# Optimization experiments

Measured on AMD Instinct MI355X. Metric: run time of the kernel, lower is better.

Reference implementation:

```python
import jax, jax.numpy as jnp
import numpy as np

EPS = 1e-5   # torch BatchNorm2d default eps
HEADS = 4


def conv1x1_bn(x, w, g, b, m, v):
    # 1x1 conv (no bias) == channel matmul, then inference-mode BatchNorm
    y = jnp.einsum('oc,bchw->bohw', w, x)
    s = g / jnp.sqrt(v + EPS)
    return y * s[None, :, None, None] + (b - m * s)[None, :, None, None]


def dwconv3x3_bn(x, w, g, b, m, v):
    # depthwise 3x3 conv, padding 1 (autopad), groups=C, then BatchNorm
    C = x.shape[1]
    y = jax.lax.conv_general_dilated(
        x, w, window_strides=(1, 1), padding=((1, 1), (1, 1)),
        dimension_numbers=('NCHW', 'OIHW', 'NCHW'), feature_group_count=C)
    s = g / jnp.sqrt(v + EPS)
    return y * s[None, :, None, None] + (b - m * s)[None, :, None, None]


def split_heads(x):
    b, c, h, w = x.shape
    hd = c // HEADS
    return x.reshape(b, HEADS, hd, h * w).transpose(0, 1, 3, 2)  # [b,heads,n,hd]


def merge_heads(x, h, w):
    b, heads, n, hd = x.shape
    return x.transpose(0, 1, 3, 2).reshape(b, heads * hd, h, w)


def setup_inputs() -> dict:
    key = jax.random.key(0)
    B, C, H, W = 4, 256, 48, 48
    ks = jax.random.split(key, 32)
    inp = {
        'q': jax.random.normal(ks[0], (B, C, H, W), jnp.float32),
        'k': jax.random.normal(ks[1], (B, C, H, W), jnp.float32),
        'v': jax.random.normal(ks[2], (B, C, H, W), jnp.float32),
    }
    i = 3
    for name in ['wq', 'wk', 'wv', 'proj']:
        inp[name + '_w'] = jax.random.normal(ks[i], (C, C), jnp.float32) * 0.02; i += 1
    inp['pe_w'] = jax.random.normal(ks[i], (C, 1, 3, 3), jnp.float32) * 0.1; i += 1
    for name in ['wq', 'wk', 'wv', 'pe', 'proj']:
        inp[name + '_g'] = jax.random.uniform(ks[i], (C,), jnp.float32, 0.5, 1.5); i += 1
        inp[name + '_b'] = jax.random.normal(ks[i], (C,), jnp.float32) * 0.1; i += 1
        inp[name + '_m'] = jax.random.normal(ks[i], (C,), jnp.float32) * 0.1; i += 1
        inp[name + '_v'] = jax.random.uniform(ks[i], (C,), jnp.float32, 0.5, 1.5); i += 1
    return inp


def reference(q, k, v,
              wq_w, wk_w, wv_w, proj_w, pe_w,
              wq_g, wq_b, wq_m, wq_v,
              wk_g, wk_b, wk_m, wk_v,
              wv_g, wv_b, wv_m, wv_v,
              pe_g, pe_b, pe_m, pe_v,
              proj_g, proj_b, proj_m, proj_v):
    H, W = q.shape[2], q.shape[3]
    qf = conv1x1_bn(q, wq_w, wq_g, wq_b, wq_m, wq_v)
    kf = conv1x1_bn(k, wk_w, wk_g, wk_b, wk_m, wk_v)
    vf = conv1x1_bn(v, wv_w, wv_g, wv_b, wv_m, wv_v)
    qh = split_heads(qf)  # [b,heads,n,hd]
    kh = split_heads(kf)
    vh = split_heads(vf)
    scale = qh.shape[-1] ** -0.5
    attn = jax.nn.softmax(jnp.einsum('bhnd,bhmd->bhnm', qh, kh) * scale, axis=-1)
    y = jnp.einsum('bhnm,bhmd->bhnd', attn, vh)
    y = merge_heads(y, H, W) + dwconv3x3_bn(merge_heads(qh, H, W), pe_w, pe_g, pe_b, pe_m, pe_v)
    return conv1x1_bn(y, proj_w, proj_g, proj_b, proj_m, proj_v)
```

## Files before the change

### kernel.cpp

```cpp
#include <hip/hip_runtime.h>
#include <math.h>

#define HEADS 4
#define HD    64
#define CCH   256
#define NB    4
#define HH    48
#define WW    48
#define NN    (HH*WW)
#define EPSBN 1e-5f
#define KSCL  0.18033688f
#define BCN   (NB*CCH*NN)
#define NSP   4

typedef unsigned short ushort_t;
typedef __attribute__((ext_vector_type(8))) short bfrag;
typedef __attribute__((ext_vector_type(4))) float f32x4;

#define MFMA __builtin_amdgcn_mfma_f32_16x16x32_bf16

static __device__ __forceinline__ ushort_t f2bf(float x) {
    unsigned int u = __float_as_uint(x);
    unsigned int r = (u + 0x7fffu + ((u >> 16) & 1u)) >> 16;
    return (ushort_t)r;
}
static __device__ __forceinline__ unsigned cvtpk(float lo, float hi) {
    unsigned r;
    asm("v_cvt_pk_bf16_f32 %0, %1, %2" : "=v"(r) : "v"(lo), "v"(hi));
    return r;
}
static __device__ __forceinline__ float bflo(unsigned u) { return __uint_as_float(u << 16); }
static __device__ __forceinline__ float bfhi(unsigned u) { return __uint_as_float(u & 0xffff0000u); }

static __device__ __forceinline__ void gload16(const void* g, void* l) {
    __builtin_amdgcn_global_load_lds(
        (const __attribute__((address_space(1))) void*)g,
        (__attribute__((address_space(3))) void*)l, 16, 0, 0);
}

struct PrepWP {
    const float* W[4];
    const float* G[4]; const float* Bb[4]; const float* Mm[4]; const float* Vv[4];
    const float* pew; const float* peg; const float* peb; const float* pem; const float* pev;
    ushort_t* W4; float* bias4; ushort_t* pw2; float* pbias; float* kmax2;
    const float* q; const float* k; const float* v; ushort_t* Xt;
};
__global__ __launch_bounds__(256)
void prep_kernel(PrepWP P)
{
    const int blk = blockIdx.x, tid = threadIdx.x;
    if (blk < 3456) {
        const int t  = blk / 1152;
        const int r  = blk % 1152;
        const int b  = r / 288;
        const int r2 = r % 288;
        const int n0 = (r2 >> 3) * 64;
        const int cb = (r2 & 7) * 32;
        const float* X = (t == 0) ? P.q : (t == 1) ? P.k : P.v;
        ushort_t* O = P.Xt + (size_t)t * BCN;
        const int lane = tid & 63;
        const int c0   = cb + (tid >> 6) * 8;
        const float* src = X + ((size_t)(b * CCH + c0) * NN + n0 + lane);
        float vv[8];
#pragma unroll
        for (int j = 0; j < 8; ++j) vv[j] = src[(size_t)j * NN];
        uint4 u;
        u.x = cvtpk(vv[0], vv[1]); u.y = cvtpk(vv[2], vv[3]);
        u.z = cvtpk(vv[4], vv[5]); u.w = cvtpk(vv[6], vv[7]);
        *(uint4*)&O[((size_t)b * NN + n0 + lane) * CCH + c0] = u;
        return;
    }
    const int wb = blk - 3456;
    if (wb == 128) {
        int c = tid;
        float s = P.peg[c] * rsqrtf(P.pev[c] + EPSBN);
        for (int tap = 0; tap < 9; ++tap)
            P.pw2[tap * CCH + c] = f2bf(P.pew[c * 9 + tap] * s);
        P.pbias[c] = P.peb[c] - P.pem[c] * s;
        if (tid < 16) P.kmax2[tid] = 0.f;
        return;
    }
    int g  = wb * 256 + tid;
    int cv = g >> 13;
    int o  = (g >> 5) & 255;
    int c8 = g & 31;
    float s  = P.G[cv][o] * rsqrtf(P.Vv[cv][o] + EPSBN);
    float s2 = (cv == 1) ? s * KSCL : s;
    const float* w = P.W[cv] + (size_t)o * CCH + c8 * 8;
    uint4 u;
    u.x = cvtpk(w[0]*s2, w[1]*s2); u.y = cvtpk(w[2]*s2, w[3]*s2);
    u.z = cvtpk(w[4]*s2, w[5]*s2); u.w = cvtpk(w[6]*s2, w[7]*s2);
    *(uint4*)&P.W4[((size_t)cv * CCH + o) * CCH + c8 * 8] = u;
    if (c8 == 0) {
        float bb = (P.Bb[cv][o] - P.Mm[cv][o] * s);
        P.bias4[cv * CCH + o] = (cv == 1) ? bb * KSCL : bb;
    }
}

template<int PROJ>
__global__ __launch_bounds__(256)
void conv_gemm(const ushort_t* __restrict__ T, const ushort_t* __restrict__ W4,
               const float* __restrict__ bias4,
               ushort_t* __restrict__ qnd, ushort_t* __restrict__ knd,
               ushort_t* __restrict__ vcn, float* __restrict__ outf,
               float* __restrict__ kmax2)
{
    __shared__ ushort_t Ts[64][264];
    __shared__ ushort_t Ws[64][264];
    const int nt = blockIdx.x, ot = blockIdx.y, z = blockIdx.z;
    const int which = PROJ ? 3 : (z >> 2);
    const int b = z & 3;
    const int tid = threadIdx.x;
    const int n0 = nt * 64, o0 = ot * 64;
    const ushort_t* Tsrc = T + (PROJ ? (size_t)0 : (size_t)which * BCN) + ((size_t)b * NN + n0) * CCH;
    const ushort_t* Wsrc = W4 + (size_t)which * CCH * CCH + (size_t)o0 * CCH;
    const float*    bias = bias4 + which * CCH;
#pragma unroll
    for (int i = 0; i < 8; ++i) {
        int idx = tid + i * 256;
        int r = idx >> 5, c16 = idx & 31;
        *(uint4*)&Ts[r][c16 * 8] = *(const uint4*)&Tsrc[(size_t)r * CCH + c16 * 8];
        *(uint4*)&Ws[r][c16 * 8] = *(const uint4*)&Wsrc[(size_t)r * CCH + c16 * 8];
    }
    __syncthreads();
    const int wv = tid >> 6, lane = tid & 63, lr = lane & 15, lg = lane >> 4;
    const int qn = (wv >> 1) * 32, qo = (wv & 1) * 32;
    f32x4 acc[2][2];
#pragma unroll
    for (int i = 0; i < 2; ++i)
#pragma unroll
        for (int j = 0; j < 2; ++j) acc[i][j] = (f32x4){0.f, 0.f, 0.f, 0.f};

    if (!PROJ && (z >> 2) < 2) {
#pragma unroll
        for (int k8 = 0; k8 < 8; ++k8) {
            const int kc = k8 * 32 + lg * 8;
            bfrag ta0 = *(const bfrag*)&Ts[qn + lr][kc];
            bfrag ta1 = *(const bfrag*)&Ts[qn + 16 + lr][kc];
            bfrag wa0 = *(const bfrag*)&Ws[qo + lr][kc];
            bfrag wa1 = *(const bfrag*)&Ws[qo + 16 + lr][kc];
            acc[0][0] = MFMA(ta0, wa0, acc[0][0], 0, 0, 0);
            acc[0][1] = MFMA(ta0, wa1, acc[0][1], 0, 0, 0);
            acc[1][0] = MFMA(ta1, wa0, acc[1][0], 0, 0, 0);
            acc[1][1] = MFMA(ta1, wa1, acc[1][1], 0, 0, 0);
        }
    } else {
#pragma unroll
        for (int k8 = 0; k8 < 8; ++k8) {
            const int kc = k8 * 32 + lg * 8;
            bfrag ta0 = *(const bfrag*)&Ts[qn + lr][kc];
            bfrag ta1 = *(const bfrag*)&Ts[qn + 16 + lr][kc];
            bfrag wa0 = *(const bfrag*)&Ws[qo + lr][kc];
            bfrag wa1 = *(const bfrag*)&Ws[qo + 16 + lr][kc];
            acc[0][0] = MFMA(wa0, ta0, acc[0][0], 0, 0, 0);
            acc[0][1] = MFMA(wa0, ta1, acc[0][1], 0, 0, 0);
            acc[1][0] = MFMA(wa1, ta0, acc[1][0], 0, 0, 0);
            acc[1][1] = MFMA(wa1, ta1, acc[1][1], 0, 0, 0);
        }
    }

    __syncthreads();
    if (!PROJ && which < 2) {
        ushort_t (*Ot)[72] = (ushort_t(*)[72])Ts;
        float bv[2] = { bias[o0 + qo + lr], bias[o0 + qo + 16 + lr] };
#pragma unroll
        for (int i = 0; i < 2; ++i)
#pragma unroll
            for (int j = 0; j < 2; ++j)
#pragma unroll
                for (int r = 0; r < 4; ++r)
                    Ot[qn + i * 16 + lg * 4 + r][qo + j * 16 + lr] = f2bf(acc[i][j][r] + bv[j]);
        __syncthreads();
        ushort_t* out = (which == 0) ? qnd : knd;
        for (int idx = tid; idx < 512; idx += 256) {
            int r = idx >> 3, sg = idx & 7;
            *(uint4*)&out[(((size_t)b * HEADS + ot) * NN + n0 + r) * HD + sg * 8] =
                *(const uint4*)&Ot[r][sg * 8];
        }
        if (which == 1 && tid < 64) {
            float s = 0.f;
#pragma unroll
            for (int j = 0; j < 8; ++j) {
                uint4 u = *(const uint4*)&Ot[tid][j * 8];
                s += bflo(u.x)*bflo(u.x) + bfhi(u.x)*bfhi(u.x);
                s += bflo(u.y)*bflo(u.y) + bfhi(u.y)*bfhi(u.y);
                s += bflo(u.z)*bflo(u.z) + bfhi(u.z)*bfhi(u.z);
                s += bflo(u.w)*bflo(u.w) + bfhi(u.w)*bfhi(u.w);
            }
            atomicMax((unsigned*)&kmax2[b * HEADS + ot], __float_as_uint(s));
        }
    } else if (!PROJ) {
        ushort_t (*Ot)[72] = (ushort_t(*)[72])Ts;
#pragma unroll
        for (int i = 0; i < 2; ++i)
#pragma unroll
            for (int r = 0; r < 4; ++r) {
                float bv = bias[o0 + qo + i * 16 + lg * 4 + r];
#pragma unroll
                for (int j = 0; j < 2; ++j)
                    Ot[qo + i * 16 + lg * 4 + r][qn + j * 16 + lr] = f2bf(acc[i][j][r] + bv);
            }
        __syncthreads();
        for (int idx = tid; idx < 512; idx += 256) {
            int r = idx >> 3, sg = idx & 7;
            *(uint4*)&vcn[((size_t)b * CCH + o0 + r) * NN + n0 + sg * 8] =
                *(const uint4*)&Ot[r][sg * 8];
        }
    } else {
        float (*Of)[68] = (float(*)[68])Ts;
#pragma unroll
        for (int i = 0; i < 2; ++i)
#pragma unroll
            for (int r = 0; r < 4; ++r) {
                float bv = bias[o0 + qo + i * 16 + lg * 4 + r];
#pragma unroll
                for (int j = 0; j < 2; ++j)
                    Of[qo + i * 16 + lg * 4 + r][qn + j * 16 + lr] = acc[i][j][r] + bv;
            }
        __syncthreads();
        for (int idx = tid; idx < 1024; idx += 256) {
            int r = idx >> 4, c4 = idx & 15;
            *(float4*)&outf[((size_t)b * CCH + o0 + r) * NN + n0 + c4 * 4] =
                *(const float4*)&Of[r][c4 * 4];
        }
    }
}

__global__ __launch_bounds__(256, 4)
void attn_kernel(const ushort_t* __restrict__ Qnd,
                 const ushort_t* __restrict__ Knd,
                 const ushort_t* __restrict__ Vcn,
                 const float* __restrict__ kmax2,
                 ushort_t* __restrict__ Op,
                 float* __restrict__ Larr)
{
    __shared__ __align__(16) char smem[40960];

    const int tid = threadIdx.x;
    const int lin0 = blockIdx.x + 18 * blockIdx.y + 288 * blockIdx.z;
    const int w    = (lin0 & 7) * 144 + (lin0 >> 3);
    const int qt = w % 18;
    const int bh = (w / 18) & 15;
    const int sp = w / 288;
    const int b = bh >> 2, h = bh & 3;
    const int lane = tid & 63, wv = tid >> 6;
    const int lr = lane & 15, lg = lane >> 4;
    const int lrow = lane >> 3, lslot = (lane & 7) ^ lrow;
    const int n0 = qt * 128;
    const size_t ndb = (size_t)(b * HEADS + h) * NN * HD;
    const size_t cnb = ((size_t)b * CCH + h * HD) * NN;

    const char* kgp = (const char*)(Knd + ndb) + (size_t)(sp * 576 + wv * 16 + lrow) * 128 + lslot * 16;
    const char* vgp = (const char*)(Vcn + cnb + sp * 576) + (size_t)(wv * 16 + lrow) * (NN * 2) + lslot * 16;
    char* kls = smem + wv * 2048;
    char* vls = smem + 16384 + wv * 2048;

#define STAGE(buf, t) do { \
    const char* kp_ = kgp + (size_t)(t) * 8192; \
    const char* vp_ = vgp + (size_t)(t) * 128; \
    char* kd_ = kls + (buf) * 8192; \
    char* vd_ = vls + (buf) * 8192; \
    gload16(kp_,              kd_); \
    gload16(kp_ + 1024,       kd_ + 1024); \
    gload16(vp_,              vd_); \
    gload16(vp_ + 8 * (NN*2), vd_ + 1024); \
} while (0)

    bfrag qb[2][2];
    {
        const ushort_t* qbase = Qnd + ndb + (size_t)(n0 + wv * 32 + lr) * HD;
        qb[0][0] = *(const bfrag*)&qbase[lg * 8];
        qb[0][1] = *(const bfrag*)&qbase[32 + lg * 8];
        qb[1][0] = *(const bfrag*)&qbase[16 * HD + lg * 8];
        qb[1][1] = *(const bfrag*)&qbase[16 * HD + 32 + lg * 8];
    }
    float m0[2];
    {
        const float kmx = sqrtf(kmax2[bh]);
#pragma unroll
        for (int qc = 0; qc < 2; ++qc) {
            const unsigned* u0 = (const unsigned*)&qb[qc][0];
            const unsigned* u1 = (const unsigned*)&qb[qc][1];
            float s = 0.f;
#pragma unroll
            for (int j = 0; j < 4; ++j) {
                float a0 = bflo(u0[j]), a1 = bfhi(u0[j]);
                float b0 = bflo(u1[j]), b1 = bfhi(u1[j]);
                s += a0*a0 + a1*a1 + b0*b0 + b1*b1;
            }
            s += __shfl_xor(s, 16);
            s += __shfl_xor(s, 32);
            m0[qc] = sqrtf(s) * kmx + 0.5f;
        }
    }
    bfrag ones_f;
    {
        short ov = (lr == 0) ? (short)0x3F80 : (short)0;
#pragma unroll
        for (int j = 0; j < 8; ++j) ones_f[j] = ov;
    }

    f32x4 o[2][4], o4[2];
#pragma unroll
    for (int qc = 0; qc < 2; ++qc) {
        o4[qc] = (f32x4){0.f, 0.f, 0.f, 0.f};
#pragma unroll
        for (int db = 0; db < 4; ++db) o[qc][db] = (f32x4){0.f, 0.f, 0.f, 0.f};
    }

    const int sw0 = (lg ^ (lr & 7)) << 4;
    const int sw1 = ((4 + lg) ^ (lr & 7)) << 4;
    char* Pw = smem + 32768 + wv * 2048;

    STAGE(0, 0);

    for (int t = 0; t < 9; ++t) {
        const int cur = t & 1;
        if (t < 8) {
            STAGE(cur ^ 1, t + 1);
            asm volatile("s_waitcnt vmcnt(4)" ::: "memory");
        } else {
            asm volatile("s_waitcnt vmcnt(0)" ::: "memory");
        }
        __builtin_amdgcn_s_barrier();
        const char* Kb = smem + cur * 8192;
        const char* Vb = smem + 16384 + cur * 8192;

        uint2 pd[2][4];
#pragma unroll
        for (int kb = 0; kb < 4; ++kb) {
            const char* krow = Kb + (kb * 16 + lr) * 128;
            bfrag ka0 = *(const bfrag*)(krow + sw0);
            bfrag ka1 = *(const bfrag*)(krow + sw1);
            __builtin_amdgcn_s_setprio(1);
            f32x4 z0 = (f32x4){-m0[0], -m0[0], -m0[0], -m0[0]};
            z0 = MFMA(ka0, qb[0][0], z0, 0, 0, 0);
            f32x4 s0 = MFMA(ka1, qb[0][1], z0, 0, 0, 0);
            f32x4 z1 = (f32x4){-m0[1], -m0[1], -m0[1], -m0[1]};
            z1 = MFMA(ka0, qb[1][0], z1, 0, 0, 0);
            f32x4 s1 = MFMA(ka1, qb[1][1], z1, 0, 0, 0);
            __builtin_amdgcn_s_setprio(0);
            pd[0][kb].x = cvtpk(exp2f(s0[0]), exp2f(s0[1]));
            pd[0][kb].y = cvtpk(exp2f(s0[2]), exp2f(s0[3]));
            pd[1][kb].x = cvtpk(exp2f(s1[0]), exp2f(s1[1]));
            pd[1][kb].y = cvtpk(exp2f(s1[2]), exp2f(s1[3]));
        }

        bfrag pb[2][2];
#pragma unroll
        for (int qc = 0; qc < 2; ++qc) {
            char* prow = Pw + lr * 128;
#pragma unroll
            for (int kb = 0; kb < 4; ++kb) {
                int slot = (2 * kb + (lg >> 1)) ^ (lr & 7);
                *(uint2*)(prow + slot * 16 + (lg & 1) * 8) = pd[qc][kb];
            }
            pb[qc][0] = *(const bfrag*)(prow + sw0);
            pb[qc][1] = *(const bfrag*)(prow + sw1);
        }

        __builtin_amdgcn_s_setprio(1);
#pragma unroll
        for (int db = 0; db < 4; ++db) {
            const char* vrow = Vb + (db * 16 + lr) * 128;
            bfrag va0 = *(const bfrag*)(vrow + sw0);
            bfrag va1 = *(const bfrag*)(vrow + sw1);
            o[0][db] = MFMA(va0, pb[0][0], o[0][db], 0, 0, 0);
            o[0][db] = MFMA(va1, pb[0][1], o[0][db], 0, 0, 0);
            o[1][db] = MFMA(va0, pb[1][0], o[1][db], 0, 0, 0);
            o[1][db] = MFMA(va1, pb[1][1], o[1][db], 0, 0, 0);
        }
        o4[0] = MFMA(ones_f, pb[0][0], o4[0], 0, 0, 0);
        o4[0] = MFMA(ones_f, pb[0][1], o4[0], 0, 0, 0);
        o4[1] = MFMA(ones_f, pb[1][0], o4[1], 0, 0, 0);
        o4[1] = MFMA(ones_f, pb[1][1], o4[1], 0, 0, 0);
        __builtin_amdgcn_s_setprio(0);

        __builtin_amdgcn_s_barrier();
    }
#undef STAGE

    if (lg == 0) {
#pragma unroll
        for (int qc = 0; qc < 2; ++qc)
            Larr[(size_t)(sp * 16 + bh) * NN + n0 + wv * 32 + qc * 16 + lr] = o4[qc][0];
    }
    unsigned (*Osb)[36] = (unsigned(*)[36])smem;
#pragma unroll
    for (int qc = 0; qc < 2; ++qc) {
        int row = wv * 32 + qc * 16 + lr;
#pragma unroll
        for (int db = 0; db < 4; ++db) {
            Osb[row][db * 8 + lg * 2 + 0] = cvtpk(o[qc][db][0], o[qc][db][1]);
            Osb[row][db * 8 + lg * 2 + 1] = cvtpk(o[qc][db][2], o[qc][db][3]);
        }
    }
    __syncthreads();
    ushort_t* opb = Op + (size_t)sp * BCN + ((size_t)b * NN + n0) * CCH + h * HD;
    for (int idx = tid; idx < 1024; idx += 256) {
        int n = idx >> 3, s4 = idx & 7;
        *(uint4*)&opb[(size_t)n * CCH + s4 * 8] = *(const uint4*)&Osb[n][s4 * 4];
    }
}

__global__ __launch_bounds__(256)
void fuse_kernel(const ushort_t* __restrict__ Op, const float* __restrict__ Larr,
                 const ushort_t* __restrict__ Qnd,
                 const ushort_t* __restrict__ pw2, const float* __restrict__ pbias,
                 ushort_t* __restrict__ yt)
{
    const int tid = threadIdx.x;
    const int b  = blockIdx.x / 288;
    const int n0 = (blockIdx.x % 288) * 8;
    const int c8 = tid & 31, ns = tid >> 5;
    const int n  = n0 + ns;
    const int h  = c8 >> 3, c0 = c8 * 8;

    const ushort_t* o0p = Op + ((size_t)b * NN + n) * CCH + c0;
    float acc[8] = {0.f, 0.f, 0.f, 0.f, 0.f, 0.f, 0.f, 0.f};
#pragma unroll
    for (int s = 0; s < NSP; ++s) {
        uint4 u = *(const uint4*)&o0p[(size_t)s * BCN];
        acc[0] += bflo(u.x); acc[1] += bfhi(u.x);
        acc[2] += bflo(u.y); acc[3] += bfhi(u.y);
        acc[4] += bflo(u.z); acc[5] += bfhi(u.z);
        acc[6] += bflo(u.w); acc[7] += bfhi(u.w);
    }
    int mi = (b * HEADS + h) * NN + n;
    float ls = 0.f;
#pragma unroll
    for (int s = 0; s < NSP; ++s) ls += Larr[(size_t)s * 16 * NN + mi];
    float rinv = 1.0f / ls;
#pragma unroll
    for (int j = 0; j < 8; ++j) acc[j] *= rinv;

    const int x = n % WW, y = n / WW;
    const ushort_t* qb = Qnd + (size_t)(b * HEADS + h) * NN * HD + (c8 & 7) * 8;
#pragma unroll
    for (int ky = 0; ky < 3; ++ky) {
        int yy = y + ky - 1;
        if (yy < 0 || yy >= HH) continue;
#pragma unroll
        for (int kx = 0; kx < 3; ++kx) {
            int xx = x + kx - 1;
            if (xx < 0 || xx >= WW) continue;
            int np = yy * WW + xx;
            uint4 qv = *(const uint4*)&qb[(size_t)np * HD];
            uint4 w4 = *(const uint4*)&pw2[(ky * 3 + kx) * CCH + c0];
            acc[0] += bflo(qv.x) * bflo(w4.x); acc[1] += bfhi(qv.x) * bfhi(w4.x);
            acc[2] += bflo(qv.y) * bflo(w4.y); acc[3] += bfhi(qv.y) * bfhi(w4.y);
            acc[4] += bflo(qv.z) * bflo(w4.z); acc[5] += bfhi(qv.z) * bfhi(w4.z);
            acc[6] += bflo(qv.w) * bflo(w4.w); acc[7] += bfhi(qv.w) * bfhi(w4.w);
        }
    }
    float4 p0 = *(const float4*)&pbias[c0];
    float4 p1 = *(const float4*)&pbias[c0 + 4];
    acc[0] += p0.x; acc[1] += p0.y; acc[2] += p0.z; acc[3] += p0.w;
    acc[4] += p1.x; acc[5] += p1.y; acc[6] += p1.z; acc[7] += p1.w;
    uint4 u;
    u.x = cvtpk(acc[0], acc[1]); u.y = cvtpk(acc[2], acc[3]);
    u.z = cvtpk(acc[4], acc[5]); u.w = cvtpk(acc[6], acc[7]);
    *(uint4*)&yt[((size_t)b * NN + n) * CCH + c0] = u;
}

extern "C" void kernel_launch(void* const* d_in, const int* in_sizes, int n_in,
                              void* d_out, int out_size, void* d_ws, size_t ws_size,
                              hipStream_t stream) {
    char* ws = (char*)d_ws;
    ushort_t* qnd  = (ushort_t*)(ws + 0);
    ushort_t* knd  = (ushort_t*)(ws + 4718592);
    ushort_t* vcn  = (ushort_t*)(ws + 9437184);
    ushort_t* Xt   = (ushort_t*)(ws + 14155776);
    ushort_t* Op   = (ushort_t*)(ws + 14155776);
    ushort_t* yt   = (ushort_t*)(ws + 4718592);
    float*    Larr = (float*)   (ws + 33030144);
    ushort_t* W4   = (ushort_t*)(ws + 33619968);
    float*    bias4= (float*)   (ws + 34144256);
    ushort_t* pw2  = (ushort_t*)(ws + 34148352);
    float*    pbias= (float*)   (ws + 34152960);
    float*    kmax2= (float*)   (ws + 34156032);

    PrepWP P;
    P.W[0] = (const float*)d_in[3]; P.W[1] = (const float*)d_in[4];
    P.W[2] = (const float*)d_in[5]; P.W[3] = (const float*)d_in[6];
    P.G[0]  = (const float*)d_in[8];  P.Bb[0] = (const float*)d_in[9];
    P.Mm[0] = (const float*)d_in[10]; P.Vv[0] = (const float*)d_in[11];
    P.G[1]  = (const float*)d_in[12]; P.Bb[1] = (const float*)d_in[13];
    P.Mm[1] = (const float*)d_in[14]; P.Vv[1] = (const float*)d_in[15];
    P.G[2]  = (const float*)d_in[16]; P.Bb[2] = (const float*)d_in[17];
    P.Mm[2] = (const float*)d_in[18]; P.Vv[2] = (const float*)d_in[19];
    P.G[3]  = (const float*)d_in[24]; P.Bb[3] = (const float*)d_in[25];
    P.Mm[3] = (const float*)d_in[26]; P.Vv[3] = (const float*)d_in[27];
    P.pew = (const float*)d_in[7];
    P.peg = (const float*)d_in[20]; P.peb = (const float*)d_in[21];
    P.pem = (const float*)d_in[22]; P.pev = (const float*)d_in[23];
    P.W4 = W4; P.bias4 = bias4; P.pw2 = pw2; P.pbias = pbias; P.kmax2 = kmax2;
    P.q = (const float*)d_in[0]; P.k = (const float*)d_in[1];
    P.v = (const float*)d_in[2]; P.Xt = Xt;

    prep_kernel<<<3585, 256, 0, stream>>>(P);

    conv_gemm<0><<<dim3(36, 4, 12), 256, 0, stream>>>(Xt, W4, bias4, qnd, knd, vcn, nullptr, kmax2);

    attn_kernel<<<dim3(18, 16, NSP), 256, 0, stream>>>(qnd, knd, vcn, kmax2, Op, Larr);

    fuse_kernel<<<1152, 256, 0, stream>>>(Op, Larr, qnd, pw2, pbias, yt);

    conv_gemm<1><<<dim3(36, 4, 4), 256, 0, stream>>>(yt, W4, bias4, nullptr, nullptr, nullptr,
                                                     (float*)d_out, nullptr);
}
```

Measured before the change: 91.89 us.

## Double attention query tile per block to reuse staged K/V tiles

Each attention block now handles 256 queries instead of 128, with each wave owning four 16-row query chunks. Every K/V tile staged into LDS therefore feeds twice as many MFMAs, halving global K/V traffic and the number of blocks (576 instead of 1152). The cost is more registers (launch bounds drop to 2 blocks per SM), 64KB of LDS, and fewer blocks to hide latency, so occupancy falls. P is now written to LDS inside the QK loop for each query chunk.

```diff
diff --git a/kernel.cpp b/kernel.cpp
--- a/kernel.cpp
+++ b/kernel.cpp
@@ -226,7 +226,7 @@
     }
 }
 
-__global__ __launch_bounds__(256, 4)
+__global__ __launch_bounds__(256, 2)
 void attn_kernel(const ushort_t* __restrict__ Qnd,
                  const ushort_t* __restrict__ Knd,
                  const ushort_t* __restrict__ Vcn,
@@ -234,19 +234,19 @@
                  ushort_t* __restrict__ Op,
                  float* __restrict__ Larr)
 {
-    __shared__ __align__(16) char smem[40960];
+    __shared__ __align__(16) char smem[65536];
 
     const int tid = threadIdx.x;
-    const int lin0 = blockIdx.x + 18 * blockIdx.y + 288 * blockIdx.z;
-    const int w    = (lin0 & 7) * 144 + (lin0 >> 3);
-    const int qt = w % 18;
-    const int bh = (w / 18) & 15;
-    const int sp = w / 288;
+    const int lin0 = blockIdx.x + 9 * blockIdx.y + 144 * blockIdx.z;
+    const int w    = (lin0 & 7) * 72 + (lin0 >> 3);
+    const int qt = w % 9;
+    const int bh = (w / 9) & 15;
+    const int sp = w / 144;
     const int b = bh >> 2, h = bh & 3;
     const int lane = tid & 63, wv = tid >> 6;
     const int lr = lane & 15, lg = lane >> 4;
     const int lrow = lane >> 3, lslot = (lane & 7) ^ lrow;
-    const int n0 = qt * 128;
+    const int n0 = qt * 256;
     const size_t ndb = (size_t)(b * HEADS + h) * NN * HD;
     const size_t cnb = ((size_t)b * CCH + h * HD) * NN;
 
@@ -266,19 +266,20 @@
     gload16(vp_ + 8 * (NN*2), vd_ + 1024); \
 } while (0)
 
-    bfrag qb[2][2];
+    bfrag qb[4][2];
     {
-        const ushort_t* qbase = Qnd + ndb + (size_t)(n0 + wv * 32 + lr) * HD;
-        qb[0][0] = *(const bfrag*)&qbase[lg * 8];
-        qb[0][1] = *(const bfrag*)&qbase[32 + lg * 8];
-        qb[1][0] = *(const bfrag*)&qbase[16 * HD + lg * 8];
-        qb[1][1] = *(const bfrag*)&qbase[16 * HD + 32 + lg * 8];
-    }
-    float m0[2];
+        const ushort_t* qbase = Qnd + ndb + (size_t)(n0 + wv * 64 + lr) * HD;
+#pragma unroll
+        for (int qc = 0; qc < 4; ++qc) {
+            qb[qc][0] = *(const bfrag*)&qbase[(size_t)qc * 16 * HD + lg * 8];
+            qb[qc][1] = *(const bfrag*)&qbase[(size_t)qc * 16 * HD + 32 + lg * 8];
+        }
+    }
+    float m0[4];
     {
         const float kmx = sqrtf(kmax2[bh]);
 #pragma unroll
-        for (int qc = 0; qc < 2; ++qc) {
+        for (int qc = 0; qc < 4; ++qc) {
             const unsigned* u0 = (const unsigned*)&qb[qc][0];
             const unsigned* u1 = (const unsigned*)&qb[qc][1];
             float s = 0.f;
@@ -300,9 +301,9 @@
         for (int j = 0; j < 8; ++j) ones_f[j] = ov;
     }
 
-    f32x4 o[2][4], o4[2];
-#pragma unroll
-    for (int qc = 0; qc < 2; ++qc) {
+    f32x4 o[4][4], o4[4];
+#pragma unroll
+    for (int qc = 0; qc < 4; ++qc) {
         o4[qc] = (f32x4){0.f, 0.f, 0.f, 0.f};
 #pragma unroll
         for (int db = 0; db < 4; ++db) o[qc][db] = (f32x4){0.f, 0.f, 0.f, 0.f};
@@ -310,7 +311,7 @@
 
     const int sw0 = (lg ^ (lr & 7)) << 4;
     const int sw1 = ((4 + lg) ^ (lr & 7)) << 4;
-    char* Pw = smem + 32768 + wv * 2048;
+    char* Pw = smem + 32768 + wv * 8192;
 
     STAGE(0, 0);
 
@@ -326,35 +327,30 @@
         const char* Kb = smem + cur * 8192;
         const char* Vb = smem + 16384 + cur * 8192;
 
-        uint2 pd[2][4];
+        __builtin_amdgcn_s_setprio(1);
 #pragma unroll
         for (int kb = 0; kb < 4; ++kb) {
             const char* krow = Kb + (kb * 16 + lr) * 128;
             bfrag ka0 = *(const bfrag*)(krow + sw0);
             bfrag ka1 = *(const bfrag*)(krow + sw1);
-            __builtin_amdgcn_s_setprio(1);
-            f32x4 z0 = (f32x4){-m0[0], -m0[0], -m0[0], -m0[0]};
-            z0 = MFMA(ka0, qb[0][0], z0, 0, 0, 0);
-            f32x4 s0 = MFMA(ka1, qb[0][1], z0, 0, 0, 0);
-            f32x4 z1 = (f32x4){-m0[1], -m0[1], -m0[1], -m0[1]};
-            z1 = MFMA(ka0, qb[1][0], z1, 0, 0, 0);
-            f32x4 s1 = MFMA(ka1, qb[1][1], z1, 0, 0, 0);
-            __builtin_amdgcn_s_setprio(0);
-            pd[0][kb].x = cvtpk(exp2f(s0[0]), exp2f(s0[1]));
-            pd[0][kb].y = cvtpk(exp2f(s0[2]), exp2f(s0[3]));
-            pd[1][kb].x = cvtpk(exp2f(s1[0]), exp2f(s1[1]));
-            pd[1][kb].y = cvtpk(exp2f(s1[2]), exp2f(s1[3]));
-        }
-
-        bfrag pb[2][2];
-#pragma unroll
-        for (int qc = 0; qc < 2; ++qc) {
-            char* prow = Pw + lr * 128;
-#pragma unroll
-            for (int kb = 0; kb < 4; ++kb) {
-                int slot = (2 * kb + (lg >> 1)) ^ (lr & 7);
-                *(uint2*)(prow + slot * 16 + (lg & 1) * 8) = pd[qc][kb];
+            const int slot = (2 * kb + (lg >> 1)) ^ (lr & 7);
+#pragma unroll
+            for (int qc = 0; qc < 4; ++qc) {
+                f32x4 z = (f32x4){-m0[qc], -m0[qc], -m0[qc], -m0[qc]};
+                z = MFMA(ka0, qb[qc][0], z, 0, 0, 0);
+                z = MFMA(ka1, qb[qc][1], z, 0, 0, 0);
+                uint2 u;
+                u.x = cvtpk(exp2f(z[0]), exp2f(z[1]));
+                u.y = cvtpk(exp2f(z[2]), exp2f(z[3]));
+                *(uint2*)(Pw + qc * 2048 + lr * 128 + slot * 16 + (lg & 1) * 8) = u;
             }
+        }
+        __builtin_amdgcn_s_setprio(0);
+
+        bfrag pb[4][2];
+#pragma unroll
+        for (int qc = 0; qc < 4; ++qc) {
+            const char* prow = Pw + qc * 2048 + lr * 128;
             pb[qc][0] = *(const bfrag*)(prow + sw0);
             pb[qc][1] = *(const bfrag*)(prow + sw1);
         }
@@ -365,15 +361,17 @@
             const char* vrow = Vb + (db * 16 + lr) * 128;
             bfrag va0 = *(const bfrag*)(vrow + sw0);
             bfrag va1 = *(const bfrag*)(vrow + sw1);
-            o[0][db] = MFMA(va0, pb[0][0], o[0][db], 0, 0, 0);
-            o[0][db] = MFMA(va1, pb[0][1], o[0][db], 0, 0, 0);
-            o[1][db] = MFMA(va0, pb[1][0], o[1][db], 0, 0, 0);
-            o[1][db] = MFMA(va1, pb[1][1], o[1][db], 0, 0, 0);
-        }
-        o4[0] = MFMA(ones_f, pb[0][0], o4[0], 0, 0, 0);
-        o4[0] = MFMA(ones_f, pb[0][1], o4[0], 0, 0, 0);
-        o4[1] = MFMA(ones_f, pb[1][0], o4[1], 0, 0, 0);
-        o4[1] = MFMA(ones_f, pb[1][1], o4[1], 0, 0, 0);
+#pragma unroll
+            for (int qc = 0; qc < 4; ++qc) {
+                o[qc][db] = MFMA(va0, pb[qc][0], o[qc][db], 0, 0, 0);
+                o[qc][db] = MFMA(va1, pb[qc][1], o[qc][db], 0, 0, 0);
+            }
+        }
+#pragma unroll
+        for (int qc = 0; qc < 4; ++qc) {
+            o4[qc] = MFMA(ones_f, pb[qc][0], o4[qc], 0, 0, 0);
+            o4[qc] = MFMA(ones_f, pb[qc][1], o4[qc], 0, 0, 0);
+        }
         __builtin_amdgcn_s_setprio(0);
 
         __builtin_amdgcn_s_barrier();
@@ -382,13 +380,13 @@
 
     if (lg == 0) {
 #pragma unroll
-        for (int qc = 0; qc < 2; ++qc)
-            Larr[(size_t)(sp * 16 + bh) * NN + n0 + wv * 32 + qc * 16 + lr] = o4[qc][0];
+        for (int qc = 0; qc < 4; ++qc)
+            Larr[(size_t)(sp * 16 + bh) * NN + n0 + wv * 64 + qc * 16 + lr] = o4[qc][0];
     }
     unsigned (*Osb)[36] = (unsigned(*)[36])smem;
 #pragma unroll
-    for (int qc = 0; qc < 2; ++qc) {
-        int row = wv * 32 + qc * 16 + lr;
+    for (int qc = 0; qc < 4; ++qc) {
+        int row = wv * 64 + qc * 16 + lr;
 #pragma unroll
         for (int db = 0; db < 4; ++db) {
             Osb[row][db * 8 + lg * 2 + 0] = cvtpk(o[qc][db][0], o[qc][db][1]);
@@ -397,7 +395,7 @@
     }
     __syncthreads();
     ushort_t* opb = Op + (size_t)sp * BCN + ((size_t)b * NN + n0) * CCH + h * HD;
-    for (int idx = tid; idx < 1024; idx += 256) {
+    for (int idx = tid; idx < 2048; idx += 256) {
         int n = idx >> 3, s4 = idx & 7;
         *(uint4*)&opb[(size_t)n * CCH + s4 * 8] = *(const uint4*)&Osb[n][s4 * 4];
     }
@@ -502,7 +500,7 @@
 
     conv_gemm<0><<<dim3(36, 4, 12), 256, 0, stream>>>(Xt, W4, bias4, qnd, knd, vcn, nullptr, kmax2);
 
-    attn_kernel<<<dim3(18, 16, NSP), 256, 0, stream>>>(qnd, knd, vcn, kmax2, Op, Larr);
+    attn_kernel<<<dim3(9, 16, NSP), 256, 0, stream>>>(qnd, knd, vcn, kmax2, Op, Larr);
 
     fuse_kernel<<<1152, 256, 0, stream>>>(Op, Larr, qnd, pw2, pbias, yt);
 
```

After: 103.6 us. 12.8% more time.

## Switch attention kernel to 32x32x16 MFMA with register-resident P via permlane32 swap

Applied to the files above, without the earlier changes.

Rewrites the attention inner loop to use 32x32x16 bf16 MFMAs instead of 16x16x32, so each wave computes scores for 32 queries against 32-key blocks. The score-to-PV operand transpose now stays in registers using v_permlane32_swap instead of a round-trip through LDS. The row sum is accumulated in scalar registers instead of a ones-vector MFMA. LDS usage drops, and redundant MFMAs and LDS traffic are removed, at the cost of more register pressure from the 16-wide accumulators.

```diff
diff --git a/kernel.cpp b/kernel.cpp
--- a/kernel.cpp
+++ b/kernel.cpp
@@ -16,8 +16,10 @@
 typedef unsigned short ushort_t;
 typedef __attribute__((ext_vector_type(8))) short bfrag;
 typedef __attribute__((ext_vector_type(4))) float f32x4;
-
-#define MFMA __builtin_amdgcn_mfma_f32_16x16x32_bf16
+typedef __attribute__((ext_vector_type(16))) float f32x16;
+
+#define MFMA   __builtin_amdgcn_mfma_f32_16x16x32_bf16
+#define MFMA32 __builtin_amdgcn_mfma_f32_32x32x16_bf16
 
 static __device__ __forceinline__ ushort_t f2bf(float x) {
     unsigned int u = __float_as_uint(x);
@@ -234,7 +236,7 @@
                  ushort_t* __restrict__ Op,
                  float* __restrict__ Larr)
 {
-    __shared__ __align__(16) char smem[40960];
+    __shared__ __align__(16) char smem[32768];
 
     const int tid = threadIdx.x;
     const int lin0 = blockIdx.x + 18 * blockIdx.y + 288 * blockIdx.z;
@@ -244,7 +246,7 @@
     const int sp = w / 288;
     const int b = bh >> 2, h = bh & 3;
     const int lane = tid & 63, wv = tid >> 6;
-    const int lr = lane & 15, lg = lane >> 4;
+    const int l31 = lane & 31, hi = lane >> 5, l7 = lane & 7;
     const int lrow = lane >> 3, lslot = (lane & 7) ^ lrow;
     const int n0 = qt * 128;
     const size_t ndb = (size_t)(b * HEADS + h) * NN * HD;
@@ -266,51 +268,35 @@
     gload16(vp_ + 8 * (NN*2), vd_ + 1024); \
 } while (0)
 
-    bfrag qb[2][2];
+    bfrag qb[4];
     {
-        const ushort_t* qbase = Qnd + ndb + (size_t)(n0 + wv * 32 + lr) * HD;
-        qb[0][0] = *(const bfrag*)&qbase[lg * 8];
-        qb[0][1] = *(const bfrag*)&qbase[32 + lg * 8];
-        qb[1][0] = *(const bfrag*)&qbase[16 * HD + lg * 8];
-        qb[1][1] = *(const bfrag*)&qbase[16 * HD + 32 + lg * 8];
-    }
-    float m0[2];
+        const ushort_t* qbase = Qnd + ndb + (size_t)(n0 + wv * 32 + l31) * HD + hi * 8;
+#pragma unroll
+        for (int ds = 0; ds < 4; ++ds)
+            qb[ds] = *(const bfrag*)&qbase[ds * 16];
+    }
+    float m0;
     {
-        const float kmx = sqrtf(kmax2[bh]);
-#pragma unroll
-        for (int qc = 0; qc < 2; ++qc) {
-            const unsigned* u0 = (const unsigned*)&qb[qc][0];
-            const unsigned* u1 = (const unsigned*)&qb[qc][1];
-            float s = 0.f;
+        float s = 0.f;
+#pragma unroll
+        for (int ds = 0; ds < 4; ++ds) {
+            const unsigned* uu = (const unsigned*)&qb[ds];
 #pragma unroll
             for (int j = 0; j < 4; ++j) {
-                float a0 = bflo(u0[j]), a1 = bfhi(u0[j]);
-                float b0 = bflo(u1[j]), b1 = bfhi(u1[j]);
-                s += a0*a0 + a1*a1 + b0*b0 + b1*b1;
-            }
-            s += __shfl_xor(s, 16);
-            s += __shfl_xor(s, 32);
-            m0[qc] = sqrtf(s) * kmx + 0.5f;
-        }
-    }
-    bfrag ones_f;
-    {
-        short ov = (lr == 0) ? (short)0x3F80 : (short)0;
-#pragma unroll
-        for (int j = 0; j < 8; ++j) ones_f[j] = ov;
-    }
-
-    f32x4 o[2][4], o4[2];
-#pragma unroll
-    for (int qc = 0; qc < 2; ++qc) {
-        o4[qc] = (f32x4){0.f, 0.f, 0.f, 0.f};
-#pragma unroll
-        for (int db = 0; db < 4; ++db) o[qc][db] = (f32x4){0.f, 0.f, 0.f, 0.f};
-    }
-
-    const int sw0 = (lg ^ (lr & 7)) << 4;
-    const int sw1 = ((4 + lg) ^ (lr & 7)) << 4;
-    char* Pw = smem + 32768 + wv * 2048;
+                float a0 = bflo(uu[j]), a1 = bfhi(uu[j]);
+                s += a0*a0 + a1*a1;
+            }
+        }
+        s += __shfl_xor(s, 32);
+        m0 = sqrtf(s) * sqrtf(kmax2[bh]) + 0.5f;
+    }
+
+    f32x16 o[2];
+#pragma unroll
+    for (int db = 0; db < 2; ++db)
+#pragma unroll
+        for (int j = 0; j < 16; ++j) o[db][j] = 0.f;
+    float lacc = 0.f;
 
     STAGE(0, 0);
 
@@ -326,74 +312,69 @@
         const char* Kb = smem + cur * 8192;
         const char* Vb = smem + 16384 + cur * 8192;
 
-        uint2 pd[2][4];
-#pragma unroll
-        for (int kb = 0; kb < 4; ++kb) {
-            const char* krow = Kb + (kb * 16 + lr) * 128;
-            bfrag ka0 = *(const bfrag*)(krow + sw0);
-            bfrag ka1 = *(const bfrag*)(krow + sw1);
+        bfrag pf[4];
+#pragma unroll
+        for (int kb = 0; kb < 2; ++kb) {
+            f32x16 s;
+#pragma unroll
+            for (int j = 0; j < 16; ++j) s[j] = -m0;
             __builtin_amdgcn_s_setprio(1);
-            f32x4 z0 = (f32x4){-m0[0], -m0[0], -m0[0], -m0[0]};
-            z0 = MFMA(ka0, qb[0][0], z0, 0, 0, 0);
-            f32x4 s0 = MFMA(ka1, qb[0][1], z0, 0, 0, 0);
-            f32x4 z1 = (f32x4){-m0[1], -m0[1], -m0[1], -m0[1]};
-            z1 = MFMA(ka0, qb[1][0], z1, 0, 0, 0);
-            f32x4 s1 = MFMA(ka1, qb[1][1], z1, 0, 0, 0);
+#pragma unroll
+            for (int ds = 0; ds < 4; ++ds) {
+                const char* ka_p = Kb + (kb * 32 + l31) * 128 + (((2 * ds + hi) ^ l7) << 4);
+                bfrag ka = *(const bfrag*)ka_p;
+                s = MFMA32(ka, qb[ds], s, 0, 0, 0);
+            }
             __builtin_amdgcn_s_setprio(0);
-            pd[0][kb].x = cvtpk(exp2f(s0[0]), exp2f(s0[1]));
-            pd[0][kb].y = cvtpk(exp2f(s0[2]), exp2f(s0[3]));
-            pd[1][kb].x = cvtpk(exp2f(s1[0]), exp2f(s1[1]));
-            pd[1][kb].y = cvtpk(exp2f(s1[2]), exp2f(s1[3]));
-        }
-
-        bfrag pb[2][2];
-#pragma unroll
-        for (int qc = 0; qc < 2; ++qc) {
-            char* prow = Pw + lr * 128;
-#pragma unroll
-            for (int kb = 0; kb < 4; ++kb) {
-                int slot = (2 * kb + (lg >> 1)) ^ (lr & 7);
-                *(uint2*)(prow + slot * 16 + (lg & 1) * 8) = pd[qc][kb];
-            }
-            pb[qc][0] = *(const bfrag*)(prow + sw0);
-            pb[qc][1] = *(const bfrag*)(prow + sw1);
+            float e[16];
+#pragma unroll
+            for (int j = 0; j < 16; ++j) { e[j] = exp2f(s[j]); lacc += e[j]; }
+            unsigned u[4][2];
+#pragma unroll
+            for (int g = 0; g < 4; ++g) {
+                u[g][0] = cvtpk(e[4 * g + 0], e[4 * g + 1]);
+                u[g][1] = cvtpk(e[4 * g + 2], e[4 * g + 3]);
+            }
+#pragma unroll
+            for (int ks = 0; ks < 2; ++ks) {
+                asm("v_permlane32_swap_b32 %0, %1" : "+v"(u[2*ks][0]), "+v"(u[2*ks+1][0]));
+                asm("v_permlane32_swap_b32 %0, %1" : "+v"(u[2*ks][1]), "+v"(u[2*ks+1][1]));
+                uint4 fw = { u[2*ks][0], u[2*ks][1], u[2*ks+1][0], u[2*ks+1][1] };
+                pf[kb * 2 + ks] = *(const bfrag*)&fw;
+            }
         }
 
         __builtin_amdgcn_s_setprio(1);
 #pragma unroll
-        for (int db = 0; db < 4; ++db) {
-            const char* vrow = Vb + (db * 16 + lr) * 128;
-            bfrag va0 = *(const bfrag*)(vrow + sw0);
-            bfrag va1 = *(const bfrag*)(vrow + sw1);
-            o[0][db] = MFMA(va0, pb[0][0], o[0][db], 0, 0, 0);
-            o[0][db] = MFMA(va1, pb[0][1], o[0][db], 0, 0, 0);
-            o[1][db] = MFMA(va0, pb[1][0], o[1][db], 0, 0, 0);
-            o[1][db] = MFMA(va1, pb[1][1], o[1][db], 0, 0, 0);
-        }
-        o4[0] = MFMA(ones_f, pb[0][0], o4[0], 0, 0, 0);
-        o4[0] = MFMA(ones_f, pb[0][1], o4[0], 0, 0, 0);
-        o4[1] = MFMA(ones_f, pb[1][0], o4[1], 0, 0, 0);
-        o4[1] = MFMA(ones_f, pb[1][1], o4[1], 0, 0, 0);
+        for (int db = 0; db < 2; ++db)
+#pragma unroll
+            for (int ks = 0; ks < 4; ++ks) {
+                const char* va_p = Vb + (db * 32 + l31) * 128 + (((2 * ks + hi) ^ l7) << 4);
+                bfrag va = *(const bfrag*)va_p;
+                o[db] = MFMA32(va, pf[ks], o[db], 0, 0, 0);
+            }
         __builtin_amdgcn_s_setprio(0);
 
         __builtin_amdgcn_s_barrier();
     }
 #undef STAGE
 
-    if (lg == 0) {
-#pragma unroll
-        for (int qc = 0; qc < 2; ++qc)
-            Larr[(size_t)(sp * 16 + bh) * NN + n0 + wv * 32 + qc * 16 + lr] = o4[qc][0];
-    }
+    lacc += __shfl_xor(lacc, 32);
+    if (hi == 0)
+        Larr[(size_t)(sp * 16 + bh) * NN + n0 + wv * 32 + l31] = lacc;
+
     unsigned (*Osb)[36] = (unsigned(*)[36])smem;
-#pragma unroll
-    for (int qc = 0; qc < 2; ++qc) {
-        int row = wv * 32 + qc * 16 + lr;
-#pragma unroll
-        for (int db = 0; db < 4; ++db) {
-            Osb[row][db * 8 + lg * 2 + 0] = cvtpk(o[qc][db][0], o[qc][db][1]);
-            Osb[row][db * 8 + lg * 2 + 1] = cvtpk(o[qc][db][2], o[qc][db][3]);
-        }
+    {
+        int row = wv * 32 + l31;
+#pragma unroll
+        for (int db = 0; db < 2; ++db)
+#pragma unroll
+            for (int g = 0; g < 4; ++g) {
+                uint2 pk;
+                pk.x = cvtpk(o[db][4 * g + 0], o[db][4 * g + 1]);
+                pk.y = cvtpk(o[db][4 * g + 2], o[db][4 * g + 3]);
+                *(uint2*)&Osb[row][16 * db + 4 * g + 2 * hi] = pk;
+            }
     }
     __syncthreads();
     ushort_t* opb = Op + (size_t)sp * BCN + ((size_t)b * NN + n0) * CCH + h * HD;
```

After: 91.66 us. Within noise of the previous version (-0.2%).
